# Kernel tuning notes

Measured on AMD Instinct MI355X. Metric: run time of the kernel, lower is better.

## Reference

```python
import jax, jax.numpy as jnp
import numpy as np
from jax import lax

A_PLUS = 0.01
A_MINUS = 0.01
TAU_PLUS = 20.0
TAU_MINUS = 20.0
W_MAX = 1.0
W_MIN = 0.0

B, T, PRE_N, POST_N = 16, 128, 2048, 2048


def setup_inputs() -> dict:
    key = jax.random.key(0)
    k1, k2, k3 = jax.random.split(key, 3)
    weights = jax.random.uniform(k1, (POST_N, PRE_N), dtype=jnp.float32)
    pre_spikes = jax.random.uniform(k2, (B, T, PRE_N), dtype=jnp.float32)
    post_spikes = jax.random.uniform(k3, (B, T, POST_N), dtype=jnp.float32)
    return {"weights": weights, "pre_spikes": pre_spikes,
            "post_spikes": post_spikes, "dt": 1}


def compute_trace(spikes, tau, dt):
    # Faithful to torch loop: trace[:,0,:] = 0; trace[t] = decay*trace[t-1] + spikes[t] for t>=1
    decay = jnp.exp(jnp.float32(-dt / tau))
    s_tb = jnp.swapaxes(spikes, 0, 1)  # [T, B, N]
    init = jnp.zeros_like(s_tb[0])

    def step(carry, s_t):
        tr = decay * carry + s_t
        return tr, tr

    _, tr = lax.scan(step, init, s_tb[1:])          # [T-1, B, N]
    tr = jnp.concatenate([init[None], tr], axis=0)  # [T, B, N]
    return jnp.swapaxes(tr, 0, 1)                   # [B, T, N]


def reference(weights, pre_spikes, post_spikes, dt):
    batch = pre_spikes.shape[0]
    pre_trace = compute_trace(pre_spikes, TAU_PLUS, dt)
    post_trace = compute_trace(post_spikes, TAU_MINUS, dt)

    # sum over t of mean over batch of outer products -> single contraction over (b, t)
    # ltp[q,p] = A_plus * sum_t mean_b post_spikes[b,t,q] * pre_trace[b,t,p]
    ltp = A_PLUS * jnp.einsum('btq,btp->qp', post_spikes, pre_trace) / batch
    # ltd[q,p] = -A_minus * sum_t mean_b post_trace[b,t,q] * pre_spikes[b,t,p]
    ltd = -A_MINUS * jnp.einsum('btq,btp->qp', post_trace, pre_spikes) / batch

    # softbound weight dependence (constant in t, distributes over the sum)
    w_factor = (W_MAX - weights) * (weights - W_MIN) / ((W_MAX - W_MIN) / 2) ** 2
    delta_w = w_factor * (ltp + ltd)
    return delta_w
```

## Files before the change

### kernel.cpp

```cpp
#include <hip/hip_runtime.h>
#include <hip/hip_bf16.h>


typedef __attribute__((ext_vector_type(8))) short bf16x8;
typedef __attribute__((ext_vector_type(4))) float f32x4;

#define GN 2048
#define KTOT 2048
#define A_SCALE (0.01f / 16.0f)

#define GLOAD_LDS16(gp, lp) \
    __builtin_amdgcn_global_load_lds((const __attribute__((address_space(1))) void*)(gp), \
                                     (__attribute__((address_space(3))) void*)(lp), 16, 0, 0)

__global__ __launch_bounds__(256) void trace_kernel(
    const float* __restrict__ pre,
    const float* __restrict__ post,
    const int* __restrict__ dtp,
    __hip_bfloat16* __restrict__ AT,
    __hip_bfloat16* __restrict__ BT)
{
    __shared__ float fbuf[128 * 65];
    __shared__ __hip_bfloat16 zbuf[128 * 65];

    const int tid = threadIdx.x;
    const int w   = tid >> 6;
    const int l   = tid & 63;
    const int n0  = blockIdx.x * 64;
    const int b   = blockIdx.y;
    const int a   = blockIdx.z;

    int di = dtp[0];
    float dtf = (di > 0 && di < 1000000) ? (float)di : *(const float*)dtp;
    const float decay = __expf(-dtf / 20.0f);

    if (a == 0) {
        #pragma unroll 8
        for (int i = 0; i < 32; ++i) {
            const int t = i * 4 + w;
            float v = post[((size_t)b * 128 + t) * GN + n0 + l];
            zbuf[t * 65 + l] = __float2bfloat16(v);
        }
        __syncthreads();
    } else {
        #pragma unroll 8
        for (int i = 0; i < 32; ++i) {
            const int t = i * 4 + w;
            fbuf[t * 65 + l] = pre[((size_t)b * 128 + t) * GN + n0 + l];
        }
        __syncthreads();

        const int t0 = 32 * w;
        float carry = 0.0f;
        #pragma unroll 8
        for (int t = 1; t < t0; ++t)
            carry = decay * carry + fbuf[t * 65 + l];
        float z[32];
        #pragma unroll
        for (int j = 0; j < 32; ++j) {
            const int t = t0 + j;
            if (t >= 1) carry = decay * carry + fbuf[t * 65 + l];
            z[j] = carry;
        }
        float bc = 0.0f;
        #pragma unroll 8
        for (int t = 127; t >= t0 + 32; --t)
            bc = decay * bc + fbuf[t * 65 + l];
        #pragma unroll
        for (int j = 31; j >= 0; --j) {
            const int t = t0 + j;
            bc = decay * bc + fbuf[t * 65 + l];
            if (t >= 1) z[j] -= bc;
        }
        #pragma unroll
        for (int j = 0; j < 32; ++j)
            zbuf[(t0 + j) * 65 + l] = __float2bfloat16(z[j]);
        __syncthreads();
    }

    __hip_bfloat16* dst = (a == 0) ? AT : BT;
    #pragma unroll
    for (int j = 0; j < 4; ++j) {
        const int c  = tid + 256 * j;
        const int n  = c >> 4;
        const int tc = c & 15;
        unsigned int vv[8];
        #pragma unroll
        for (int i = 0; i < 8; ++i)
            vv[i] = *(const unsigned short*)&zbuf[(8 * tc + i) * 65 + n];
        uint4 pk;
        pk.x = vv[0] | (vv[1] << 16);
        pk.y = vv[2] | (vv[3] << 16);
        pk.z = vv[4] | (vv[5] << 16);
        pk.w = vv[6] | (vv[7] << 16);
        *(uint4*)(dst + (size_t)(n0 + n) * KTOT + b * 128 + tc * 8) = pk;
    }
}

__global__ __launch_bounds__(256) void stdp_gemm(
    const __hip_bfloat16* __restrict__ AT,
    const __hip_bfloat16* __restrict__ BT,
    float* __restrict__ out0,
    float* __restrict__ out1,
    int klen)
{
    __shared__ alignas(16) __hip_bfloat16 As[128 * 64];
    __shared__ alignas(16) __hip_bfloat16 Bs[64 * 64];

    const int tid  = threadIdx.x;
    const int lane = tid & 63;
    const int wv   = tid >> 6;
    const int wm   = (wv >> 1) * 64;
    const int wn   = (wv & 1) * 32;
    const int RM   = blockIdx.y * 128;
    const int CN   = blockIdx.x * 64;
    const int K0   = blockIdx.z * klen;
    const int l15  = lane & 15;
    const int quad = lane >> 4;

    f32x4 acc[4][2] = {};

    for (int k0 = K0; k0 < K0 + klen; k0 += 64) {
        __syncthreads();
        #pragma unroll
        for (int it = 0; it < 4; ++it) {
            const int cbase = it * 256 + wv * 64;
            const int c     = cbase + lane;
            const int row   = c >> 3;
            const int kc    = (c & 7) ^ (row & 7);
            GLOAD_LDS16(AT + (size_t)(RM + row) * KTOT + k0 + kc * 8, As + (size_t)cbase * 8);
        }
        #pragma unroll
        for (int it = 0; it < 2; ++it) {
            const int cbase = it * 256 + wv * 64;
            const int c     = cbase + lane;
            const int row   = c >> 3;
            const int kc    = (c & 7) ^ (row & 7);
            GLOAD_LDS16(BT + (size_t)(CN + row) * KTOT + k0 + kc * 8, Bs + (size_t)cbase * 8);
        }
        __syncthreads();

        #pragma unroll
        for (int kk = 0; kk < 64; kk += 32) {
            const int jg = (kk >> 3) + quad;
            bf16x8 af[4], bfr[2];
            #pragma unroll
            for (int i = 0; i < 4; ++i) {
                const int mr = wm + i * 16 + l15;
                af[i] = *(const bf16x8*)(As + mr * 64 + ((jg ^ (mr & 7)) * 8));
            }
            #pragma unroll
            for (int j = 0; j < 2; ++j) {
                const int nr = wn + j * 16 + l15;
                bfr[j] = *(const bf16x8*)(Bs + nr * 64 + ((jg ^ (nr & 7)) * 8));
            }
            #pragma unroll
            for (int i = 0; i < 4; ++i)
                #pragma unroll
                for (int j = 0; j < 2; ++j)
                    acc[i][j] = __builtin_amdgcn_mfma_f32_16x16x32_bf16(
                        af[i], bfr[j], acc[i][j], 0, 0, 0);
        }
    }

    float* outp = (blockIdx.z == 0) ? out0 : out1;
    #pragma unroll
    for (int i = 0; i < 4; ++i) {
        #pragma unroll
        for (int r = 0; r < 4; ++r) {
            const int q = RM + wm + i * 16 + quad * 4 + r;
            #pragma unroll
            for (int j = 0; j < 2; ++j) {
                const int p = CN + wn + j * 16 + l15;
                outp[(size_t)q * GN + p] = acc[i][j][r];
            }
        }
    }
}

__global__ __launch_bounds__(256) void combine_kernel(
    const float4* __restrict__ W,
    const float4* __restrict__ P1,
    float4* __restrict__ out)
{
    const size_t i = (size_t)blockIdx.x * 256 + threadIdx.x;
    float4 w = W[i];
    float4 a = out[i];
    float4 b = P1[i];
    float4 o;
    o.x = 4.0f * w.x * (1.0f - w.x) * A_SCALE * (a.x + b.x);
    o.y = 4.0f * w.y * (1.0f - w.y) * A_SCALE * (a.y + b.y);
    o.z = 4.0f * w.z * (1.0f - w.z) * A_SCALE * (a.z + b.z);
    o.w = 4.0f * w.w * (1.0f - w.w) * A_SCALE * (a.w + b.w);
    out[i] = o;
}

extern "C" void kernel_launch(void* const* d_in, const int* in_sizes, int n_in,
                              void* d_out, int out_size, void* d_ws, size_t ws_size,
                              hipStream_t stream) {
    const float* W    = (const float*)d_in[0];
    const float* pre  = (const float*)d_in[1];
    const float* post = (const float*)d_in[2];
    const int*   dt   = (const int*)d_in[3];
    float* out = (float*)d_out;

    __hip_bfloat16* AT = (__hip_bfloat16*)d_ws;
    __hip_bfloat16* BT = AT + (size_t)GN * KTOT;
    float* P1 = (float*)((char*)d_ws + (size_t)16 * 1024 * 1024);

    trace_kernel<<<dim3(32, 16, 2), 256, 0, stream>>>(pre, post, dt, AT, BT);
    stdp_gemm<<<dim3(32, 16, 2), 256, 0, stream>>>(AT, BT, out, P1, KTOT / 2);
    combine_kernel<<<4096, 256, 0, stream>>>((const float4*)W, (const float4*)P1,
                                             (float4*)out);
}
```

Measured before the change: 128.7 us.

## Fuse softbound combine into GEMM epilogue, drop split-K, vectorize trace loads

The GEMM no longer splits K across two blocks writing partial outputs. It uses 64x64 tiles over the full K with 1024 blocks, and the weight-factor scaling is applied directly in the epilogue, which removes the separate combine kernel and the partial-buffer round trip. The trace kernel now loads inputs as float4 with padded LDS strides. Each block now does a longer serial K loop with a smaller tile, so arithmetic intensity per block drops.

```diff
diff --git a/kernel.cpp b/kernel.cpp
--- a/kernel.cpp
+++ b/kernel.cpp
@@ -8,10 +8,17 @@
 #define GN 2048
 #define KTOT 2048
 #define A_SCALE (0.01f / 16.0f)
+#define FST 68
+#define ZST 66
 
 #define GLOAD_LDS16(gp, lp) \
     __builtin_amdgcn_global_load_lds((const __attribute__((address_space(1))) void*)(gp), \
                                      (__attribute__((address_space(3))) void*)(lp), 16, 0, 0)
+
+__device__ __forceinline__ unsigned bf16bits(float x) {
+    __hip_bfloat16 h = __float2bfloat16(x);
+    return (unsigned)*(unsigned short*)&h;
+}
 
 __global__ __launch_bounds__(256) void trace_kernel(
     const float* __restrict__ pre,
@@ -20,12 +27,14 @@
     __hip_bfloat16* __restrict__ AT,
     __hip_bfloat16* __restrict__ BT)
 {
-    __shared__ float fbuf[128 * 65];
-    __shared__ __hip_bfloat16 zbuf[128 * 65];
+    __shared__ float fbuf[128 * FST];
+    __shared__ __hip_bfloat16 zbuf[128 * ZST];
 
     const int tid = threadIdx.x;
     const int w   = tid >> 6;
     const int l   = tid & 63;
+    const int nq  = tid & 15;
+    const int tl  = tid >> 4;
     const int n0  = blockIdx.x * 64;
     const int b   = blockIdx.y;
     const int a   = blockIdx.z;
@@ -35,18 +44,22 @@
     const float decay = __expf(-dtf / 20.0f);
 
     if (a == 0) {
-        #pragma unroll 8
-        for (int i = 0; i < 32; ++i) {
-            const int t = i * 4 + w;
-            float v = post[((size_t)b * 128 + t) * GN + n0 + l];
-            zbuf[t * 65 + l] = __float2bfloat16(v);
+        #pragma unroll
+        for (int pass = 0; pass < 8; ++pass) {
+            const int t = pass * 16 + tl;
+            float4 v = *(const float4*)&post[((size_t)b * 128 + t) * GN + n0 + 4 * nq];
+            uint2 pk;
+            pk.x = bf16bits(v.x) | (bf16bits(v.y) << 16);
+            pk.y = bf16bits(v.z) | (bf16bits(v.w) << 16);
+            *(uint2*)&zbuf[t * ZST + 4 * nq] = pk;
         }
         __syncthreads();
     } else {
-        #pragma unroll 8
-        for (int i = 0; i < 32; ++i) {
-            const int t = i * 4 + w;
-            fbuf[t * 65 + l] = pre[((size_t)b * 128 + t) * GN + n0 + l];
+        #pragma unroll
+        for (int pass = 0; pass < 8; ++pass) {
+            const int t = pass * 16 + tl;
+            float4 v = *(const float4*)&pre[((size_t)b * 128 + t) * GN + n0 + 4 * nq];
+            *(float4*)&fbuf[t * FST + 4 * nq] = v;
         }
         __syncthreads();
 
@@ -54,27 +67,27 @@
         float carry = 0.0f;
         #pragma unroll 8
         for (int t = 1; t < t0; ++t)
-            carry = decay * carry + fbuf[t * 65 + l];
+            carry = decay * carry + fbuf[t * FST + l];
         float z[32];
         #pragma unroll
         for (int j = 0; j < 32; ++j) {
             const int t = t0 + j;
-            if (t >= 1) carry = decay * carry + fbuf[t * 65 + l];
+            if (t >= 1) carry = decay * carry + fbuf[t * FST + l];
             z[j] = carry;
         }
         float bc = 0.0f;
         #pragma unroll 8
         for (int t = 127; t >= t0 + 32; --t)
-            bc = decay * bc + fbuf[t * 65 + l];
+            bc = decay * bc + fbuf[t * FST + l];
         #pragma unroll
         for (int j = 31; j >= 0; --j) {
             const int t = t0 + j;
-            bc = decay * bc + fbuf[t * 65 + l];
+            bc = decay * bc + fbuf[t * FST + l];
             if (t >= 1) z[j] -= bc;
         }
         #pragma unroll
         for (int j = 0; j < 32; ++j)
-            zbuf[(t0 + j) * 65 + l] = __float2bfloat16(z[j]);
+            zbuf[(t0 + j) * ZST + l] = __float2bfloat16(z[j]);
         __syncthreads();
     }
 
@@ -87,7 +100,7 @@
         unsigned int vv[8];
         #pragma unroll
         for (int i = 0; i < 8; ++i)
-            vv[i] = *(const unsigned short*)&zbuf[(8 * tc + i) * 65 + n];
+            vv[i] = *(const unsigned short*)&zbuf[(8 * tc + i) * ZST + n];
         uint4 pk;
         pk.x = vv[0] | (vv[1] << 16);
         pk.y = vv[2] | (vv[3] << 16);
@@ -100,42 +113,33 @@
 __global__ __launch_bounds__(256) void stdp_gemm(
     const __hip_bfloat16* __restrict__ AT,
     const __hip_bfloat16* __restrict__ BT,
-    float* __restrict__ out0,
-    float* __restrict__ out1,
-    int klen)
+    const float* __restrict__ W,
+    float* __restrict__ out)
 {
-    __shared__ alignas(16) __hip_bfloat16 As[128 * 64];
+    __shared__ alignas(16) __hip_bfloat16 As[64 * 64];
     __shared__ alignas(16) __hip_bfloat16 Bs[64 * 64];
 
     const int tid  = threadIdx.x;
     const int lane = tid & 63;
     const int wv   = tid >> 6;
-    const int wm   = (wv >> 1) * 64;
+    const int wm   = (wv >> 1) * 32;
     const int wn   = (wv & 1) * 32;
-    const int RM   = blockIdx.y * 128;
+    const int RM   = blockIdx.y * 64;
     const int CN   = blockIdx.x * 64;
-    const int K0   = blockIdx.z * klen;
     const int l15  = lane & 15;
     const int quad = lane >> 4;
 
-    f32x4 acc[4][2] = {};
+    f32x4 acc[2][2] = {};
 
-    for (int k0 = K0; k0 < K0 + klen; k0 += 64) {
+    for (int k0 = 0; k0 < KTOT; k0 += 64) {
         __syncthreads();
-        #pragma unroll
-        for (int it = 0; it < 4; ++it) {
-            const int cbase = it * 256 + wv * 64;
-            const int c     = cbase + lane;
-            const int row   = c >> 3;
-            const int kc    = (c & 7) ^ (row & 7);
-            GLOAD_LDS16(AT + (size_t)(RM + row) * KTOT + k0 + kc * 8, As + (size_t)cbase * 8);
-        }
         #pragma unroll
         for (int it = 0; it < 2; ++it) {
             const int cbase = it * 256 + wv * 64;
             const int c     = cbase + lane;
             const int row   = c >> 3;
             const int kc    = (c & 7) ^ (row & 7);
+            GLOAD_LDS16(AT + (size_t)(RM + row) * KTOT + k0 + kc * 8, As + (size_t)cbase * 8);
             GLOAD_LDS16(BT + (size_t)(CN + row) * KTOT + k0 + kc * 8, Bs + (size_t)cbase * 8);
         }
         __syncthreads();
@@ -143,19 +147,16 @@
         #pragma unroll
         for (int kk = 0; kk < 64; kk += 32) {
             const int jg = (kk >> 3) + quad;
-            bf16x8 af[4], bfr[2];
+            bf16x8 af[2], bfr[2];
             #pragma unroll
-            for (int i = 0; i < 4; ++i) {
+            for (int i = 0; i < 2; ++i) {
                 const int mr = wm + i * 16 + l15;
                 af[i] = *(const bf16x8*)(As + mr * 64 + ((jg ^ (mr & 7)) * 8));
+                const int nr = wn + i * 16 + l15;
+                bfr[i] = *(const bf16x8*)(Bs + nr * 64 + ((jg ^ (nr & 7)) * 8));
             }
             #pragma unroll
-            for (int j = 0; j < 2; ++j) {
-                const int nr = wn + j * 16 + l15;
-                bfr[j] = *(const bf16x8*)(Bs + nr * 64 + ((jg ^ (nr & 7)) * 8));
-            }
-            #pragma unroll
-            for (int i = 0; i < 4; ++i)
+            for (int i = 0; i < 2; ++i)
                 #pragma unroll
                 for (int j = 0; j < 2; ++j)
                     acc[i][j] = __builtin_amdgcn_mfma_f32_16x16x32_bf16(
@@ -163,36 +164,20 @@
         }
     }
 
-    float* outp = (blockIdx.z == 0) ? out0 : out1;
     #pragma unroll
-    for (int i = 0; i < 4; ++i) {
+    for (int i = 0; i < 2; ++i) {
         #pragma unroll
         for (int r = 0; r < 4; ++r) {
             const int q = RM + wm + i * 16 + quad * 4 + r;
             #pragma unroll
             for (int j = 0; j < 2; ++j) {
                 const int p = CN + wn + j * 16 + l15;
-                outp[(size_t)q * GN + p] = acc[i][j][r];
+                const float w  = W[(size_t)q * GN + p];
+                const float wf = 4.0f * w * (1.0f - w);
+                out[(size_t)q * GN + p] = wf * A_SCALE * acc[i][j][r];
             }
         }
     }
-}
-
-__global__ __launch_bounds__(256) void combine_kernel(
-    const float4* __restrict__ W,
-    const float4* __restrict__ P1,
-    float4* __restrict__ out)
-{
-    const size_t i = (size_t)blockIdx.x * 256 + threadIdx.x;
-    float4 w = W[i];
-    float4 a = out[i];
-    float4 b = P1[i];
-    float4 o;
-    o.x = 4.0f * w.x * (1.0f - w.x) * A_SCALE * (a.x + b.x);
-    o.y = 4.0f * w.y * (1.0f - w.y) * A_SCALE * (a.y + b.y);
-    o.z = 4.0f * w.z * (1.0f - w.z) * A_SCALE * (a.z + b.z);
-    o.w = 4.0f * w.w * (1.0f - w.w) * A_SCALE * (a.w + b.w);
-    out[i] = o;
 }
 
 extern "C" void kernel_launch(void* const* d_in, const int* in_sizes, int n_in,
@@ -206,10 +191,7 @@
 
     __hip_bfloat16* AT = (__hip_bfloat16*)d_ws;
     __hip_bfloat16* BT = AT + (size_t)GN * KTOT;
-    float* P1 = (float*)((char*)d_ws + (size_t)16 * 1024 * 1024);
 
     trace_kernel<<<dim3(32, 16, 2), 256, 0, stream>>>(pre, post, dt, AT, BT);
-    stdp_gemm<<<dim3(32, 16, 2), 256, 0, stream>>>(AT, BT, out, P1, KTOT / 2);
-    combine_kernel<<<4096, 256, 0, stream>>>((const float4*)W, (const float4*)P1,
-                                             (float4*)out);
+    stdp_gemm<<<dim3(32, 32), 256, 0, stream>>>(AT, BT, W, out);
 }
```

New measurement: 123.2 us. -4.3%, faster.
